# Kernel tuning notes

Measured on AMD Instinct MI355X. Metric: run time of the kernel, lower is better.

## Reference

```python
import jax, jax.numpy as jnp
import numpy as np

NUM_GROUPS = 32
EPS = 1e-6


def group_norm(x, scale, bias):
    # x: [b, c, l]
    b, c, l = x.shape
    xg = x.reshape(b, NUM_GROUPS, (c // NUM_GROUPS) * l)
    mean = jnp.mean(xg, axis=2, keepdims=True)
    var = jnp.var(xg, axis=2, keepdims=True)
    xn = ((xg - mean) * jax.lax.rsqrt(var + EPS)).reshape(b, c, l)
    return xn * scale[None, :, None] + bias[None, :, None]


def conv1x1(x, w, b):
    # pointwise conv: w [out_c, in_c], x [b, in_c, l]
    return jnp.einsum('oc,bcl->bol', w, x) + b[None, :, None]


def setup_inputs() -> dict:
    key = jax.random.key(0)
    ks = jax.random.split(key, 11)
    b, c, l = 4, 512, 4096
    s = 1.0 / np.sqrt(c)
    return {
        'x': jax.random.normal(ks[0], (b, c, l), jnp.float32),
        'gn_scale': jnp.ones((c,), jnp.float32),
        'gn_bias': jnp.zeros((c,), jnp.float32),
        'wq': jax.random.normal(ks[1], (c, c), jnp.float32) * s,
        'bq': jnp.zeros((c,), jnp.float32),
        'wk': jax.random.normal(ks[2], (c, c), jnp.float32) * s,
        'bk': jnp.zeros((c,), jnp.float32),
        'wv': jax.random.normal(ks[3], (c, c), jnp.float32) * s,
        'bv': jnp.zeros((c,), jnp.float32),
        'wp': jax.random.normal(ks[4], (c, c), jnp.float32) * s,
        'bp': jnp.zeros((c,), jnp.float32),
    }


def reference(x, gn_scale, gn_bias, wq, bq, wk, bk, wv, bv, wp, bp):
    h_ = group_norm(x, gn_scale, gn_bias)
    q = conv1x1(h_, wq, bq)  # [b, c, l]
    k = conv1x1(h_, wk, bk)
    v = conv1x1(h_, wv, bv)
    c = q.shape[1]
    # scores w[b,i,j] = sum_c q[b,c,i] k[b,c,j] * c^-0.5, softmax over j
    w = jnp.einsum('bci,bcj->bij', q, k) * (c ** -0.5)
    w = jax.nn.softmax(w, axis=2)
    # out[b,c,i] = sum_j w[b,i,j] v[b,c,j]
    h_ = jnp.einsum('bij,bcj->bci', w, v)
    h_ = conv1x1(h_, wp, bp)
    return x + h_
```

## Files before the change

### kernel.cpp

```cpp
#include <hip/hip_runtime.h>
#include <math.h>

#define BB 4
#define CC 512
#define LL 4096
#define NG 32
#define CPG 16
#define EPSV 1e-6f

typedef short s16x8 __attribute__((ext_vector_type(8)));
typedef __bf16 bf8v __attribute__((ext_vector_type(8)));
typedef float f32x4 __attribute__((ext_vector_type(4)));
typedef float f32x16 __attribute__((ext_vector_type(16)));
typedef int i32x4 __attribute__((ext_vector_type(4)));
typedef int i32x8 __attribute__((ext_vector_type(8)));
typedef unsigned short u16;
typedef unsigned char u8;

typedef const __attribute__((address_space(1))) void g1_void;
typedef __attribute__((address_space(3))) void l3_void;

#define ASM_SBAR() asm volatile("s_barrier" ::: "memory")
#define ASM_WAITV(N) asm volatile("s_waitcnt vmcnt(" #N ")" ::: "memory")

static __device__ __forceinline__ float bf2f(u16 h) {
    unsigned int u = ((unsigned int)h) << 16;
    union { unsigned int u; float f; } c; c.u = u; return c.f;
}
static __device__ __forceinline__ u16 f2bf(float f) {
    union { float f; unsigned int u; } c; c.f = f;
    unsigned int lsb = (c.u >> 16) & 1u;
    c.u += 0x7fffu + lsb;
    return (u16)(c.u >> 16);
}
static __device__ __forceinline__ u8 f2fp8(float f) {
    int v = __builtin_amdgcn_cvt_pk_fp8_f32(f, f, 0, false);
    return (u8)(v & 0xff);
}
static __device__ __forceinline__ bf8v ld_bf8(const u16* p) {
    return *reinterpret_cast<const bf8v*>(p);
}
static __device__ __forceinline__ i32x8 ld32(const u8* plo, const u8* phi) {
    i32x4 lo = *reinterpret_cast<const i32x4*>(plo);
    i32x4 hi = *reinterpret_cast<const i32x4*>(phi);
    return __builtin_shufflevector(lo, hi, 0, 1, 2, 3, 4, 5, 6, 7);
}
#define MFMA_SC(a, b, c) \
    __builtin_amdgcn_mfma_scale_f32_32x32x64_f8f6f4(a, b, c, 0, 0, 0, 0x7f, 0, 0x7f)

static __device__ __forceinline__ void gload16(const u16* g, u16* l) {
    __builtin_amdgcn_global_load_lds((g1_void*)g, (l3_void*)l, 16, 0, 0);
}
static __device__ __forceinline__ void gload16b(const u8* g, u8* l) {
    __builtin_amdgcn_global_load_lds((g1_void*)g, (l3_void*)l, 16, 0, 0);
}

__global__ __launch_bounds__(256) void wconv_kernel(const float* __restrict__ w0,
                                                    const float* __restrict__ w1,
                                                    const float* __restrict__ w2,
                                                    const float* __restrict__ w3,
                                                    u16* __restrict__ wbf) {
    int i = blockIdx.x * 256 + threadIdx.x;
    int wsel = blockIdx.y;
    const float* src = (wsel == 0) ? w0 : (wsel == 1) ? w1 : (wsel == 2) ? w2 : w3;
    float4 v = reinterpret_cast<const float4*>(src)[i];
    ushort4 o;
    o.x = f2bf(v.x); o.y = f2bf(v.y); o.z = f2bf(v.z); o.w = f2bf(v.w);
    reinterpret_cast<ushort4*>(wbf + (size_t)wsel * CC * CC)[i] = o;
}

__global__ __launch_bounds__(256) void biascat_kernel(const float* __restrict__ bq,
                                                      const float* __restrict__ bk,
                                                      const float* __restrict__ bv,
                                                      float* __restrict__ bcat,
                                                      float* __restrict__ rowsum) {
    int i = blockIdx.x * 256 + threadIdx.x;
    if (i < 3 * CC) {
        float v = (i < CC) ? bq[i] : (i < 2 * CC ? bk[i - CC] : bv[i - 2 * CC]);
        bcat[i] = v;
    }
    if (i < BB * LL) rowsum[i] = 0.f;
}

__global__ __launch_bounds__(256) void gn_stats_kernel(const float* __restrict__ x,
                                                       float2* __restrict__ stats) {
    int g = blockIdx.x, b = blockIdx.y, t = threadIdx.x;
    const float4* xp = reinterpret_cast<const float4*>(x + ((size_t)b * CC + (size_t)g * CPG) * LL);
    float s = 0.f, ss = 0.f;
    for (int it = 0; it < 64; ++it) {
        float4 v = xp[it * 256 + t];
        s += v.x + v.y + v.z + v.w;
        ss += v.x * v.x + v.y * v.y + v.z * v.z + v.w * v.w;
    }
    #pragma unroll
    for (int off = 32; off; off >>= 1) { s += __shfl_xor(s, off, 64); ss += __shfl_xor(ss, off, 64); }
    __shared__ float rs[4], rss[4];
    int wave = t >> 6, lane = t & 63;
    if (lane == 0) { rs[wave] = s; rss[wave] = ss; }
    __syncthreads();
    if (t == 0) {
        float S = rs[0] + rs[1] + rs[2] + rs[3];
        float SS = rss[0] + rss[1] + rss[2] + rss[3];
        float mean = S * (1.f / 65536.f);
        float var = SS * (1.f / 65536.f) - mean * mean;
        var = fmaxf(var, 0.f);
        stats[b * NG + g] = make_float2(mean, rsqrtf(var + EPSV));
    }
}

__global__ __launch_bounds__(256) void gn_norm_t_kernel(const float* __restrict__ x,
                                                        const float2* __restrict__ stats,
                                                        const float* __restrict__ gsc,
                                                        const float* __restrict__ gbi,
                                                        u16* __restrict__ hT) {
    int lt = blockIdx.x, ct = blockIdx.y, b = blockIdx.z;
    __shared__ u16 tile[64][72];
    int t = threadIdx.x;
    int cl0 = t >> 4, c4 = (t & 15) * 4;
    #pragma unroll
    for (int p = 0; p < 4; ++p) {
        int cl = p * 16 + cl0;
        int cg = ct * 64 + cl;
        float2 st = stats[b * NG + (cg >> 4)];
        float sc = gsc[cg] * st.y;
        float bi = gbi[cg];
        float4 v = *reinterpret_cast<const float4*>(x + ((size_t)b * CC + cg) * LL + lt * 64 + c4);
        tile[cl][c4 + 0] = f2bf((v.x - st.x) * sc + bi);
        tile[cl][c4 + 1] = f2bf((v.y - st.x) * sc + bi);
        tile[cl][c4 + 2] = f2bf((v.z - st.x) * sc + bi);
        tile[cl][c4 + 3] = f2bf((v.w - st.x) * sc + bi);
    }
    __syncthreads();
    int r = t >> 3, c8 = (t & 7) * 8;
    #pragma unroll
    for (int p = 0; p < 2; ++p) {
        int ll = p * 32 + r;
        s16x8 ov;
        #pragma unroll
        for (int j = 0; j < 8; ++j) ov[j] = (short)tile[c8 + j][ll];
        u16* hp = hT + ((size_t)b * LL + lt * 64 + ll) * CC + ct * 64 + c8;
        *reinterpret_cast<s16x8*>(hp) = ov;
    }
}

template <int MODE>
__global__ __launch_bounds__(256) void gemm_kernel(const u16* __restrict__ A, size_t asb, int lda,
                                                   const u16* __restrict__ B, size_t bsb, int ldb,
                                                   const float* __restrict__ bias,
                                                   u8* __restrict__ Oq, u8* __restrict__ Ok,
                                                   u8* __restrict__ Ov, size_t osb,
                                                   const float* __restrict__ xres,
                                                   float* __restrict__ fout, int K) {
    __shared__ u16 pool[24576];
    u8* pool8 = (u8*)pool;
    int mt = blockIdx.x, nt = blockIdx.y, b = blockIdx.z;
    int t = threadIdx.x;
    int wave = t >> 6, lane = t & 63;
    int wm = (wave >> 1) * 64, wn = (wave & 1) * 64;
    int l15 = lane & 15, quad = lane >> 4;
    f32x4 acc[4][4] = {};
    const u16* Ab = A + (size_t)b * asb + (size_t)mt * 128 * lda;
    const u16* Bb = B + (size_t)b * bsb + (size_t)nt * 128 * ldb;
    int swzg = ((lane & 3) ^ ((lane >> 2) & 3) ^ ((lane >> 4) & 3)) * 8;
    int row0 = wave * 16 + (lane >> 2);
    int row1 = 64 + row0;
    const u16* Ap0 = Ab + (size_t)row0 * lda + swzg;
    const u16* Ap1 = Ab + (size_t)row1 * lda + swzg;
    const u16* Bp0 = Bb + (size_t)row0 * ldb + swzg;
    const u16* Bp1 = Bb + (size_t)row1 * ldb + swzg;
    int wo = wave * 512;
    int swzf = (l15 & 3) ^ (l15 >> 2);
    int aoff = (wm + l15) * 32 + ((quad ^ swzf) * 8);
    int boff = (wn + l15) * 32 + ((quad ^ swzf) * 8);
    const int iters = K >> 5;
    gload16(Ap0, pool + wo);                gload16(Ap1, pool + 2048 + wo);
    gload16(Bp0, pool + 12288 + wo);        gload16(Bp1, pool + 12288 + 2048 + wo);
    gload16(Ap0 + 32, pool + 4096 + wo);    gload16(Ap1 + 32, pool + 4096 + 2048 + wo);
    gload16(Bp0 + 32, pool + 16384 + wo);   gload16(Bp1 + 32, pool + 16384 + 2048 + wo);
    int bs = 0;
    for (int i = 0; i < iters; ++i) {
        if (i + 1 < iters) { ASM_WAITV(4); } else { ASM_WAITV(0); }
        ASM_SBAR();
        const u16* As = pool + bs;
        const u16* Bs = pool + 12288 + bs;
        bf8v af[4], bfr[4];
        #pragma unroll
        for (int ii = 0; ii < 4; ++ii)
            af[ii] = ld_bf8(&As[aoff + ii * 512]);
        #pragma unroll
        for (int j = 0; j < 4; ++j)
            bfr[j] = ld_bf8(&Bs[boff + j * 512]);
        if (i + 2 < iters) {
            int kk = (i + 2) * 32;
            int nb = bs + 8192; if (nb >= 12288) nb -= 12288;
            u16* as = pool + nb; u16* bsp = pool + 12288 + nb;
            gload16(Ap0 + kk, as + wo);        gload16(Ap1 + kk, as + 2048 + wo);
            gload16(Bp0 + kk, bsp + wo);       gload16(Bp1 + kk, bsp + 2048 + wo);
        }
        __builtin_amdgcn_s_setprio(1);
        #pragma unroll
        for (int ii = 0; ii < 4; ++ii)
            #pragma unroll
            for (int j = 0; j < 4; ++j)
                acc[ii][j] = __builtin_amdgcn_mfma_f32_16x16x32_bf16(af[ii], bfr[j], acc[ii][j], 0, 0, 0);
        __builtin_amdgcn_s_setprio(0);
        bs += 4096; if (bs >= 12288) bs -= 12288;
    }
    if (MODE == 0) {
        int nt_sel = nt >> 2, ntl = nt & 3;
        if (nt_sel == 2) {
            __syncthreads();
            #pragma unroll
            for (int j = 0; j < 4; ++j) {
                float bv = bias[nt * 128 + wn + j * 16 + l15];
                #pragma unroll
                for (int i = 0; i < 4; ++i) {
                    int col = wn + j * 16 + l15;
                    int row = wm + i * 16 + quad * 4;
                    unsigned int w = __builtin_amdgcn_cvt_pk_fp8_f32(acc[i][j][0] + bv, acc[i][j][1] + bv, 0, false);
                    w = __builtin_amdgcn_cvt_pk_fp8_f32(acc[i][j][2] + bv, acc[i][j][3] + bv, w, true);
                    *reinterpret_cast<unsigned int*>(&pool8[col * 144 + row]) = w;
                }
            }
            __syncthreads();
            u8* Ob = Ov + (size_t)b * osb + (size_t)(ntl * 128) * LL + mt * 128;
            #pragma unroll
            for (int it = 0; it < 4; ++it) {
                int idx = it * 256 + t;
                int row = idx >> 3, ch = (idx & 7) * 16;
                *reinterpret_cast<float4*>(Ob + (size_t)row * LL + ch) =
                    *reinterpret_cast<const float4*>(&pool8[row * 144 + ch]);
            }
        } else {
            u8* Oc = (nt_sel == 0 ? Oq : Ok) + (size_t)b * osb
                     + (size_t)(mt * 128) * CC + ntl * 128 + wn + l15;
            #pragma unroll
            for (int j = 0; j < 4; ++j) {
                float bv = bias[nt * 128 + wn + j * 16 + l15];
                #pragma unroll
                for (int i = 0; i < 4; ++i)
                    #pragma unroll
                    for (int r = 0; r < 4; ++r) {
                        int row = wm + i * 16 + quad * 4 + r;
                        Oc[(size_t)row * CC + j * 16] = f2fp8(acc[i][j][r] + bv);
                    }
            }
        }
    } else {
        __syncthreads();
        #pragma unroll
        for (int j = 0; j < 4; ++j) {
            float bv = bias[nt * 128 + wn + j * 16 + l15];
            #pragma unroll
            for (int i = 0; i < 4; ++i)
                #pragma unroll
                for (int r = 0; r < 4; ++r) {
                    int row = wm + i * 16 + quad * 4 + r;
                    int col = wn + j * 16 + l15;
                    pool[col * 136 + row] = f2bf(acc[i][j][r] + bv);
                }
        }
        __syncthreads();
        const float* xb = xres + ((size_t)b * CC + nt * 128) * LL + mt * 128;
        float* ob = fout + ((size_t)b * CC + nt * 128) * LL + mt * 128;
        #pragma unroll
        for (int it = 0; it < 16; ++it) {
            int idx = it * 256 + t;
            int cl = idx >> 5, ch = (idx & 31) * 4;
            short4 pv = *reinterpret_cast<const short4*>(&pool[cl * 136 + ch]);
            float4 xv = *reinterpret_cast<const float4*>(xb + (size_t)cl * LL + ch);
            float4 ov;
            ov.x = xv.x + bf2f((u16)pv.x);
            ov.y = xv.y + bf2f((u16)pv.y);
            ov.z = xv.z + bf2f((u16)pv.z);
            ov.w = xv.w + bf2f((u16)pv.w);
            *reinterpret_cast<float4*>(ob + (size_t)cl * LL + ch) = ov;
        }
    }
}

template <int MODE>
__global__ __launch_bounds__(256) void gemm8_kernel(const u8* __restrict__ A, size_t asb, int lda,
                                                    const u8* __restrict__ B, size_t bsb, int ldb,
                                                    float scale,
                                                    u8* __restrict__ Out8, u16* __restrict__ OutH,
                                                    size_t osb, int Nout, int K,
                                                    float* __restrict__ rsum) {
    __shared__ u8 pool8[49152];
    int mt = blockIdx.x, nt = blockIdx.y, b = blockIdx.z;
    int t = threadIdx.x;
    int wave = t >> 6, lane = t & 63;
    int wm = (wave >> 1) * 64, wn = (wave & 1) * 64;
    int l31 = lane & 31, hsel = lane >> 5;
    f32x16 acc[2][2] = {};
    int R = wave * 32 + (lane >> 1);
    int c16 = ((lane & 1) ^ (R & 1) ^ ((R >> 2) & 1)) * 16;
    const u8* Ap = A + (size_t)b * asb + (size_t)(mt * 128 + R) * lda + c16;
    const u8* Bp = B + (size_t)b * bsb + (size_t)(nt * 128 + R) * ldb + c16;
    int wo = wave * 1024;
    int ra = wm + l31;
    int rb = wn + l31;
    int sa = (ra & 1) ^ ((ra >> 2) & 1);
    int sb = (rb & 1) ^ ((rb >> 2) & 1);
    int a_lo = hsel * 4096 + ra * 32 + sa * 16;
    int a_hi = hsel * 4096 + ra * 32 + 16 - sa * 16;
    int b_lo = hsel * 4096 + rb * 32 + sb * 16;
    int b_hi = hsel * 4096 + rb * 32 + 16 - sb * 16;
    const int iters = K >> 6;
    #define STG(ii, bsv) do { int kk = (ii) * 64;                          \
        gload16b(Ap + kk,      pool8 + (bsv) + wo);                        \
        gload16b(Ap + kk + 32, pool8 + (bsv) + 4096 + wo);                 \
        gload16b(Bp + kk,      pool8 + 24576 + (bsv) + wo);                \
        gload16b(Bp + kk + 32, pool8 + 24576 + (bsv) + 4096 + wo); } while (0)
    STG(0, 0);
    STG(1, 8192);
    int bs = 0;
    for (int i = 0; i < iters; ++i) {
        if (i + 1 < iters) { ASM_WAITV(4); } else { ASM_WAITV(0); }
        ASM_SBAR();
        const u8* As = pool8 + bs;
        const u8* Bs = pool8 + 24576 + bs;
        i32x8 a0 = ld32(As + a_lo, As + a_hi);
        i32x8 a1 = ld32(As + 1024 + a_lo, As + 1024 + a_hi);
        i32x8 b0 = ld32(Bs + b_lo, Bs + b_hi);
        i32x8 b1 = ld32(Bs + 1024 + b_lo, Bs + 1024 + b_hi);
        if (i + 2 < iters) {
            int nb = bs + 16384; if (nb >= 24576) nb -= 24576;
            STG(i + 2, nb);
        }
        __builtin_amdgcn_s_setprio(1);
        acc[0][0] = MFMA_SC(a0, b0, acc[0][0]);
        acc[0][1] = MFMA_SC(a0, b1, acc[0][1]);
        acc[1][0] = MFMA_SC(a1, b0, acc[1][0]);
        acc[1][1] = MFMA_SC(a1, b1, acc[1][1]);
        __builtin_amdgcn_s_setprio(0);
        bs += 8192; if (bs >= 24576) bs -= 24576;
    }
    #undef STG
    if (MODE == 1) {
        u8* Ob = Out8 + (size_t)b * osb + (size_t)(mt * 128) * Nout + nt * 128 + wn + l31;
        float* rbase = rsum + (size_t)b * LL + mt * 128;
        #pragma unroll
        for (int i = 0; i < 2; ++i) {
            #pragma unroll
            for (int rg = 0; rg < 4; ++rg) {
                #pragma unroll
                for (int rr = 0; rr < 4; ++rr) {
                    int reg = rg * 4 + rr;
                    int row = wm + i * 32 + rr + 8 * rg + 4 * hsel;
                    float v0 = __expf(acc[i][0][reg] * scale - 3.0f);
                    float v1 = __expf(acc[i][1][reg] * scale - 3.0f);
                    u8* rp = Ob + (size_t)row * Nout;
                    rp[0]  = f2fp8(v0);
                    rp[32] = f2fp8(v1);
                    float part = v0 + v1;
                    part += __shfl_xor(part, 1, 64);
                    part += __shfl_xor(part, 2, 64);
                    part += __shfl_xor(part, 4, 64);
                    part += __shfl_xor(part, 8, 64);
                    part += __shfl_xor(part, 16, 64);
                    if (l31 == 0)
                        atomicAdd(rbase + row, part);
                }
            }
        }
    } else {
        __syncthreads();
        u16* poolh = (u16*)pool8;
        const float* rbase = rsum + (size_t)b * LL + mt * 128;
        #pragma unroll
        for (int i = 0; i < 2; ++i)
            #pragma unroll
            for (int rg = 0; rg < 4; ++rg) {
                int row0 = wm + i * 32 + 8 * rg + 4 * hsel;
                float4 rv = *reinterpret_cast<const float4*>(rbase + row0);
                float iv[4] = {1.f / rv.x, 1.f / rv.y, 1.f / rv.z, 1.f / rv.w};
                #pragma unroll
                for (int rr = 0; rr < 4; ++rr) {
                    int reg = rg * 4 + rr;
                    int row = row0 + rr;
                    poolh[row * 136 + wn + l31]      = f2bf(acc[i][0][reg] * iv[rr]);
                    poolh[row * 136 + wn + 32 + l31] = f2bf(acc[i][1][reg] * iv[rr]);
                }
            }
        __syncthreads();
        u16* Ob = OutH + (size_t)b * osb + (size_t)(mt * 128) * Nout + nt * 128;
        #pragma unroll
        for (int it = 0; it < 8; ++it) {
            int idx = it * 256 + t;
            int row = idx >> 4, ch = (idx & 15) * 8;
            s16x8 val = *reinterpret_cast<const s16x8*>(&poolh[row * 136 + ch]);
            *reinterpret_cast<s16x8*>(Ob + (size_t)row * Nout + ch) = val;
        }
    }
}

extern "C" void kernel_launch(void* const* d_in, const int* in_sizes, int n_in,
                              void* d_out, int out_size, void* d_ws, size_t ws_size,
                              hipStream_t stream) {
    const float* x   = (const float*)d_in[0];
    const float* gsc = (const float*)d_in[1];
    const float* gbi = (const float*)d_in[2];
    const float* wq  = (const float*)d_in[3];
    const float* bq  = (const float*)d_in[4];
    const float* wk  = (const float*)d_in[5];
    const float* bk  = (const float*)d_in[6];
    const float* wv  = (const float*)d_in[7];
    const float* bv  = (const float*)d_in[8];
    const float* wp  = (const float*)d_in[9];
    const float* bp  = (const float*)d_in[10];
    float* out = (float*)d_out;

    char* ws = (char*)d_ws;
    const size_t SZ   = (size_t)BB * LL * CC * 2;
    const size_t QSZ  = (size_t)BB * LL * CC;
    const size_t WQSZ = (size_t)4 * CC * CC * 2;
    const size_t RSZ  = (size_t)BB * LL * 4;
    u16* bufA = (u16*)(ws);
    u8*  q8   = (u8*)(ws + SZ);
    u8*  k8   = (u8*)(ws + SZ + QSZ);
    u8*  v8   = (u8*)(ws + SZ + 2 * QSZ);
    u16* wbf  = (u16*)(ws + SZ + 3 * QSZ);
    float2* stats = (float2*)(ws + SZ + 3 * QSZ + WQSZ);
    float* bcat   = (float*)(ws + SZ + 3 * QSZ + WQSZ + 4096);
    float* rowsum = (float*)(ws + SZ + 3 * QSZ + WQSZ + 4096 + 8192);
    u8* S8 = (u8*)(ws + SZ + 3 * QSZ + WQSZ + 4096 + 8192 + RSZ);
    const float scale = 0.044194173824159216f;
    const size_t BLC = (size_t)LL * CC;

    wconv_kernel<<<dim3(256, 4), 256, 0, stream>>>(wq, wk, wv, wp, wbf);
    biascat_kernel<<<dim3(64), 256, 0, stream>>>(bq, bk, bv, bcat, rowsum);
    gn_stats_kernel<<<dim3(NG, BB), 256, 0, stream>>>(x, stats);
    gn_norm_t_kernel<<<dim3(64, 8, BB), 256, 0, stream>>>(x, stats, gsc, gbi, bufA);
    gemm_kernel<0><<<dim3(32, 12, BB), 256, 0, stream>>>(bufA, BLC, CC, wbf, 0, CC, bcat,
                                                         q8, k8, v8, BLC, nullptr, nullptr, CC);
    gemm8_kernel<1><<<dim3(32, 32, BB), 256, 0, stream>>>(q8, BLC, CC, k8, BLC, CC, scale,
                                                          S8, nullptr, (size_t)LL * LL, LL, CC, rowsum);
    gemm8_kernel<2><<<dim3(32, 4, BB), 256, 0, stream>>>(S8, (size_t)LL * LL, LL, v8, BLC, LL, 1.f,
                                                         nullptr, bufA, BLC, CC, LL, rowsum);
    gemm_kernel<3><<<dim3(32, 4, BB), 256, 0, stream>>>(bufA, BLC, CC, wbf + 3 * CC * CC, 0, CC,
                                                        bp, nullptr, nullptr, nullptr, 0, x, out, CC);
}
```

Before: 309.7 us.

## Make each QK^T block compute four column tiles sequentially, reusing Q rows

The score GEMM grid shrinks from 32 to 8 blocks along N. Each block now loops over four 128-wide key tiles, 32 k-steps in total, and writes exp/fp8 results plus row-sum atomics after every 8 steps before zeroing its accumulators. This gives fewer blocks and lets the epilogue of one tile overlap with loads already issued for the next. It also re-reads the A tile once per sub-tile, and the in-loop epilogue raises register pressure and adds a serial stall inside the pipeline.

```diff
diff --git a/kernel.cpp b/kernel.cpp
--- a/kernel.cpp
+++ b/kernel.cpp
@@ -293,10 +293,12 @@
     int wm = (wave >> 1) * 64, wn = (wave & 1) * 64;
     int l31 = lane & 31, hsel = lane >> 5;
     f32x16 acc[2][2] = {};
+    const f32x16 fzero = {};
     int R = wave * 32 + (lane >> 1);
     int c16 = ((lane & 1) ^ (R & 1) ^ ((R >> 2) & 1)) * 16;
     const u8* Ap = A + (size_t)b * asb + (size_t)(mt * 128 + R) * lda + c16;
-    const u8* Bp = B + (size_t)b * bsb + (size_t)(nt * 128 + R) * ldb + c16;
+    const u8* Bp = B + (size_t)b * bsb
+                 + (size_t)((MODE == 1 ? nt * 512 : nt * 128) + R) * ldb + c16;
     int wo = wave * 1024;
     int ra = wm + l31;
     int rb = wn + l31;
@@ -306,15 +308,23 @@
     int a_hi = hsel * 4096 + ra * 32 + 16 - sa * 16;
     int b_lo = hsel * 4096 + rb * 32 + sb * 16;
     int b_hi = hsel * 4096 + rb * 32 + 16 - sb * 16;
-    const int iters = K >> 6;
-    #define STG(ii, bsv) do { int kk = (ii) * 64;                          \
-        gload16b(Ap + kk,      pool8 + (bsv) + wo);                        \
-        gload16b(Ap + kk + 32, pool8 + (bsv) + 4096 + wo);                 \
-        gload16b(Bp + kk,      pool8 + 24576 + (bsv) + wo);                \
-        gload16b(Bp + kk + 32, pool8 + 24576 + (bsv) + 4096 + wo); } while (0)
+    const int iters = (MODE == 1) ? 32 : (K >> 6);
+    #define STG(ii, bsv) do {                                                        \
+        size_t ao_ = (MODE == 1) ? (size_t)(((ii) & 7) * 64) : (size_t)(ii) * 64;    \
+        size_t bo_ = (MODE == 1) ? ((size_t)((ii) >> 3) * 128 * ldb + ((ii) & 7) * 64)\
+                                 : (size_t)(ii) * 64;                                \
+        gload16b(Ap + ao_,      pool8 + (bsv) + wo);                                 \
+        gload16b(Ap + ao_ + 32, pool8 + (bsv) + 4096 + wo);                          \
+        gload16b(Bp + bo_,      pool8 + 24576 + (bsv) + wo);                         \
+        gload16b(Bp + bo_ + 32, pool8 + 24576 + (bsv) + 4096 + wo); } while (0)
     STG(0, 0);
     STG(1, 8192);
     int bs = 0;
+    u8* Ob1 = nullptr; float* rbase = nullptr;
+    if (MODE == 1) {
+        Ob1 = Out8 + (size_t)b * osb + (size_t)(mt * 128) * Nout + nt * 512 + wn + l31;
+        rbase = rsum + (size_t)b * LL + mt * 128;
+    }
     for (int i = 0; i < iters; ++i) {
         if (i + 1 < iters) { ASM_WAITV(4); } else { ASM_WAITV(0); }
         ASM_SBAR();
@@ -335,45 +345,48 @@
         acc[1][1] = MFMA_SC(a1, b1, acc[1][1]);
         __builtin_amdgcn_s_setprio(0);
         bs += 8192; if (bs >= 24576) bs -= 24576;
+        if (MODE == 1 && (i & 7) == 7) {
+            int s = i >> 3;
+            u8* Obs = Ob1 + s * 128;
+            #pragma unroll
+            for (int ii = 0; ii < 2; ++ii) {
+                #pragma unroll
+                for (int rg = 0; rg < 4; ++rg) {
+                    #pragma unroll
+                    for (int rr = 0; rr < 4; ++rr) {
+                        int reg = rg * 4 + rr;
+                        int row = wm + ii * 32 + rr + 8 * rg + 4 * hsel;
+                        float v0 = __expf(acc[ii][0][reg] * scale - 3.0f);
+                        float v1 = __expf(acc[ii][1][reg] * scale - 3.0f);
+                        u8* rp = Obs + (size_t)row * Nout;
+                        rp[0]  = f2fp8(v0);
+                        rp[32] = f2fp8(v1);
+                        float part = v0 + v1;
+                        part += __shfl_xor(part, 1, 64);
+                        part += __shfl_xor(part, 2, 64);
+                        part += __shfl_xor(part, 4, 64);
+                        part += __shfl_xor(part, 8, 64);
+                        part += __shfl_xor(part, 16, 64);
+                        if (l31 == 0)
+                            atomicAdd(rbase + row, part);
+                    }
+                }
+                acc[ii][0] = fzero;
+                acc[ii][1] = fzero;
+            }
+        }
     }
     #undef STG
-    if (MODE == 1) {
-        u8* Ob = Out8 + (size_t)b * osb + (size_t)(mt * 128) * Nout + nt * 128 + wn + l31;
-        float* rbase = rsum + (size_t)b * LL + mt * 128;
-        #pragma unroll
-        for (int i = 0; i < 2; ++i) {
-            #pragma unroll
-            for (int rg = 0; rg < 4; ++rg) {
-                #pragma unroll
-                for (int rr = 0; rr < 4; ++rr) {
-                    int reg = rg * 4 + rr;
-                    int row = wm + i * 32 + rr + 8 * rg + 4 * hsel;
-                    float v0 = __expf(acc[i][0][reg] * scale - 3.0f);
-                    float v1 = __expf(acc[i][1][reg] * scale - 3.0f);
-                    u8* rp = Ob + (size_t)row * Nout;
-                    rp[0]  = f2fp8(v0);
-                    rp[32] = f2fp8(v1);
-                    float part = v0 + v1;
-                    part += __shfl_xor(part, 1, 64);
-                    part += __shfl_xor(part, 2, 64);
-                    part += __shfl_xor(part, 4, 64);
-                    part += __shfl_xor(part, 8, 64);
-                    part += __shfl_xor(part, 16, 64);
-                    if (l31 == 0)
-                        atomicAdd(rbase + row, part);
-                }
-            }
-        }
-    } else {
+    if (MODE == 2) {
         __syncthreads();
         u16* poolh = (u16*)pool8;
-        const float* rbase = rsum + (size_t)b * LL + mt * 128;
+        const float* rbase2 = rsum + (size_t)b * LL + mt * 128;
         #pragma unroll
         for (int i = 0; i < 2; ++i)
             #pragma unroll
             for (int rg = 0; rg < 4; ++rg) {
                 int row0 = wm + i * 32 + 8 * rg + 4 * hsel;
-                float4 rv = *reinterpret_cast<const float4*>(rbase + row0);
+                float4 rv = *reinterpret_cast<const float4*>(rbase2 + row0);
                 float iv[4] = {1.f / rv.x, 1.f / rv.y, 1.f / rv.z, 1.f / rv.w};
                 #pragma unroll
                 for (int rr = 0; rr < 4; ++rr) {
@@ -434,8 +447,8 @@
     gn_norm_t_kernel<<<dim3(64, 8, BB), 256, 0, stream>>>(x, stats, gsc, gbi, bufA);
     gemm_kernel<0><<<dim3(32, 12, BB), 256, 0, stream>>>(bufA, BLC, CC, wbf, 0, CC, bcat,
                                                          q8, k8, v8, BLC, nullptr, nullptr, CC);
-    gemm8_kernel<1><<<dim3(32, 32, BB), 256, 0, stream>>>(q8, BLC, CC, k8, BLC, CC, scale,
-                                                          S8, nullptr, (size_t)LL * LL, LL, CC, rowsum);
+    gemm8_kernel<1><<<dim3(32, 8, BB), 256, 0, stream>>>(q8, BLC, CC, k8, BLC, CC, scale,
+                                                         S8, nullptr, (size_t)LL * LL, LL, CC, rowsum);
     gemm8_kernel<2><<<dim3(32, 4, BB), 256, 0, stream>>>(S8, (size_t)LL * LL, LL, v8, BLC, LL, 1.f,
                                                          nullptr, bufA, BLC, CC, LL, rowsum);
     gemm_kernel<3><<<dim3(32, 4, BB), 256, 0, stream>>>(bufA, BLC, CC, wbf + 3 * CC * CC, 0, CC,
```

New measurement: 320.2 us. 1.03x slower.
